# Kernel tuning notes

Measured on AMD Instinct MI355X. Metric: run time of the kernel, lower is better.

The kernel has to match this reference:

```python
import jax, jax.numpy as jnp
import numpy as np

B, S, D, H = 2, 2048, 1024, 16
HD = D // H  # head_dim = 64
LN_EPS = 1e-5


def setup_inputs() -> dict:
    key = jax.random.key(0)
    ks = jax.random.split(key, 14)
    w = 0.02  # weight init scale
    return {
        "q": jax.random.normal(ks[0], (B, S, D), jnp.float32),
        "k": jax.random.normal(ks[1], (B, S, D), jnp.float32),
        "v": jax.random.normal(ks[2], (B, S, D), jnp.float32),
        "mask": jnp.zeros((B, 1, S, S), dtype=bool),
        "training": 0,
        "wq_w": jax.random.normal(ks[3], (D, D), jnp.float32) * w,
        "wq_b": jnp.zeros((D,), jnp.float32),
        "wk_w": jax.random.normal(ks[4], (D, D), jnp.float32) * w,
        "wk_b": jnp.zeros((D,), jnp.float32),
        "wv_w": jax.random.normal(ks[5], (D, D), jnp.float32) * w,
        "wv_b": jnp.zeros((D,), jnp.float32),
        "wo_w": jax.random.normal(ks[6], (D, D), jnp.float32) * w,
        "wo_b": jnp.zeros((D,), jnp.float32),
        "ln_g": jnp.ones((D,), jnp.float32),
        "ln_b": jnp.zeros((D,), jnp.float32),
    }


def _linear(x, w, b):
    # torch nn.Linear: x @ W.T + b, W is [out, in]
    return jnp.einsum('bsd,od->bso', x, w) + b


def _split_heads(x):
    b, s, _ = x.shape
    return x.reshape(b, s, H, HD).transpose(0, 2, 1, 3)  # [B,H,S,HD]


def reference(q, k, v, mask, training, wq_w, wq_b, wk_w, wk_b, wv_w, wv_b,
              wo_w, wo_b, ln_g, ln_b):
    residual = q
    Q = _split_heads(_linear(q, wq_w, wq_b))
    K = _split_heads(_linear(k, wk_w, wk_b))
    V = _split_heads(_linear(v, wv_w, wv_b))
    # source computes sqrt(dk) in float16, then adds 1e-8
    dk = jnp.sqrt(jnp.asarray(HD, jnp.float16)).astype(jnp.float32) + 1e-8
    score = jnp.einsum('bhqd,bhkd->bhqk', Q, K) / dk  # [B,H,S,S]
    # NOTE: source applies NO softmax; masked score is used directly.
    attn = jnp.where(mask, -jnp.inf, score)
    ctx = jnp.einsum('bhqk,bhkd->bhqd', attn, V)  # [B,H,S,HD]
    b, _, s, _ = ctx.shape
    ctx = ctx.transpose(0, 2, 1, 3).reshape(b, s, D)  # [B,S,D]
    o = _linear(ctx, wo_w, wo_b)
    # dropout is identity in eval mode
    x = residual + o
    mu = jnp.mean(x, axis=-1, keepdims=True)
    var = jnp.mean(jnp.square(x - mu), axis=-1, keepdims=True)
    return ln_g * (x - mu) * jax.lax.rsqrt(var + LN_EPS) + ln_b
```

## Files before the change

### kernel.cpp

```cpp
#include <hip/hip_runtime.h>


typedef __bf16 bf16;
typedef __bf16 bf16x8 __attribute__((ext_vector_type(8)));
typedef float f32x4 __attribute__((ext_vector_type(4)));

#define MFMA16(a, b, c) __builtin_amdgcn_mfma_f32_16x16x32_bf16(a, b, c, 0, 0, 0)
#define BARRIER() asm volatile("s_barrier" ::: "memory")
#define VMCNT6() asm volatile("s_waitcnt vmcnt(6)" ::: "memory")
#define VMCNT4() asm volatile("s_waitcnt vmcnt(4)" ::: "memory")
#define VMCNT0() asm volatile("s_waitcnt vmcnt(0)" ::: "memory")
#define LGKM0()                                        \
  do {                                                 \
    asm volatile("s_waitcnt lgkmcnt(0)" ::: "memory"); \
    __builtin_amdgcn_sched_barrier(0);                 \
  } while (0)

__device__ __forceinline__ bf16x8 ld8(const bf16* p) { return *(const bf16x8*)p; }

__device__ __forceinline__ void gload16(const void* g, void* l) {
  __builtin_amdgcn_global_load_lds((__attribute__((address_space(1))) void*)(g),
                                   (__attribute__((address_space(3))) void*)(l), 16, 0, 0);
}

__device__ __forceinline__ int swz4(int row) { return (row ^ (row >> 2)) & 3; }

__global__ __launch_bounds__(256) void wcvt_kernel(
    const float* __restrict__ wq, const float* __restrict__ wk, const float* __restrict__ wv,
    bf16* __restrict__ dst, float* __restrict__ Mz) {
  const int bid = blockIdx.x;
  if (bid >= 1536) {
    float* p = Mz + (size_t)(bid - 1536) * 2048 + threadIdx.x * 8;
    *(f32x4*)p = f32x4{0.f, 0.f, 0.f, 0.f};
    *(f32x4*)(p + 4) = f32x4{0.f, 0.f, 0.f, 0.f};
    return;
  }
  const int y = bid >> 9, x = bid & 511;
  const float* s = (y == 0) ? wq : (y == 1 ? wk : wv);
  const size_t i = ((size_t)x * 256 + threadIdx.x) * 8;
  f32x4 a = *(const f32x4*)(s + i);
  f32x4 b = *(const f32x4*)(s + i + 4);
  bf16x8 o;
  o[0] = (bf16)a[0]; o[1] = (bf16)a[1]; o[2] = (bf16)a[2]; o[3] = (bf16)a[3];
  o[4] = (bf16)b[0]; o[5] = (bf16)b[1]; o[6] = (bf16)b[2]; o[7] = (bf16)b[3];
  *(bf16x8*)(dst + (size_t)y * 1048576u + i) = o;
}

__global__ __launch_bounds__(256, 3) void gemm_proj_a(
    const float* __restrict__ q, const float* __restrict__ k, const float* __restrict__ v,
    const bf16* __restrict__ Wall,
    const float* __restrict__ bq, const float* __restrict__ bk, const float* __restrict__ bv,
    bf16* __restrict__ Call) {
  __shared__ __align__(1024) char lds[49152];
  const int wg = blockIdx.x;
  const int swz = (wg & 7) * 96 + (wg >> 3);
  const int mt = swz >> 3, nt = swz & 7;
  const int z = mt >> 5;
  const int mloc = (mt & 31) * 128;
  const int n0 = nt * 128;
  const float* As = (z == 0) ? q : (z == 1 ? k : v);
  const bf16* W = Wall + (size_t)z * 1048576u + (size_t)n0 * 1024;

  const int t = threadIdx.x;
  const int lane = t & 63, wid = t >> 6;
  const int wr = wid >> 1, wc = wid & 1;
  const int r16 = lane & 15, kg = lane >> 4;

  int aoff[4], boff[4];
#pragma unroll
  for (int i = 0; i < 4; i++) {
    const int arow = wr * 64 + i * 16 + r16;
    aoff[i] = arow * 64 + ((kg ^ swz4(arow)) << 4);
    const int brow = wc * 64 + i * 16 + r16;
    boff[i] = brow * 64 + ((kg ^ swz4(brow)) << 4);
  }

  const int ar = t >> 1;
  const float* Arow = As + (size_t)(mloc + ar) * 1024 + (t & 1) * 16;
  const int ws0 = ar * 64 + (((((t & 1) << 1) | 0) ^ swz4(ar)) << 4);
  const int ws1 = ar * 64 + (((((t & 1) << 1) | 1) ^ swz4(ar)) << 4);

  const int c1 = t, c2 = t + 256;
  const bf16* pb1 = W + (size_t)(c1 >> 2) * 1024 + ((c1 & 3) ^ swz4(c1 >> 2)) * 8;
  const bf16* pb2 = W + (size_t)(c2 >> 2) * 1024 + ((c2 & 3) ^ swz4(c2 >> 2)) * 8;
  const int bd1 = wid << 10, bd2 = 4096 + (wid << 10);

  f32x4 rg0, rg1, rg2, rg3;
  f32x4 acc[4][4] = {};

  {
    const float* p = Arow;
    rg0 = *(const f32x4*)p; rg1 = *(const f32x4*)(p + 4);
    rg2 = *(const f32x4*)(p + 8); rg3 = *(const f32x4*)(p + 12);
  }
  __builtin_amdgcn_sched_barrier(0);
  gload16(pb1, lds + 24576 + bd1);
  gload16(pb2, lds + 24576 + bd2);
  gload16(pb1 + 32, lds + 24576 + 8192 + bd1);
  gload16(pb2 + 32, lds + 24576 + 8192 + bd2);
  {
    bf16x8 p0, p1;
    p0[0] = (bf16)rg0[0]; p0[1] = (bf16)rg0[1]; p0[2] = (bf16)rg0[2]; p0[3] = (bf16)rg0[3];
    p0[4] = (bf16)rg1[0]; p0[5] = (bf16)rg1[1]; p0[6] = (bf16)rg1[2]; p0[7] = (bf16)rg1[3];
    p1[0] = (bf16)rg2[0]; p1[1] = (bf16)rg2[1]; p1[2] = (bf16)rg2[2]; p1[3] = (bf16)rg2[3];
    p1[4] = (bf16)rg3[0]; p1[5] = (bf16)rg3[1]; p1[6] = (bf16)rg3[2]; p1[7] = (bf16)rg3[3];
    *(bf16x8*)(lds + ws0) = p0;
    *(bf16x8*)(lds + ws1) = p1;
  }
  {
    const float* p = Arow + 32;
    rg0 = *(const f32x4*)p; rg1 = *(const f32x4*)(p + 4);
    rg2 = *(const f32x4*)(p + 8); rg3 = *(const f32x4*)(p + 12);
  }
  LGKM0();
  VMCNT6();
  BARRIER();

  int cb = 0;
  for (int kt = 0; kt < 32; ++kt) {
    const char* la = lds + cb * 8192;
    const char* lb = lds + 24576 + cb * 8192;
    bf16x8 av[4], bw[4];
#pragma unroll
    for (int i = 0; i < 4; i++) av[i] = *(const bf16x8*)(la + aoff[i]);
#pragma unroll
    for (int j = 0; j < 4; j++) bw[j] = *(const bf16x8*)(lb + boff[j]);

    const int nb = (cb == 2) ? 0 : cb + 1;
    const int pbuf = (nb == 2) ? 0 : nb + 1;
    if (kt < 31) {
      bf16x8 p0, p1;
      p0[0] = (bf16)rg0[0]; p0[1] = (bf16)rg0[1]; p0[2] = (bf16)rg0[2]; p0[3] = (bf16)rg0[3];
      p0[4] = (bf16)rg1[0]; p0[5] = (bf16)rg1[1]; p0[6] = (bf16)rg1[2]; p0[7] = (bf16)rg1[3];
      p1[0] = (bf16)rg2[0]; p1[1] = (bf16)rg2[1]; p1[2] = (bf16)rg2[2]; p1[3] = (bf16)rg2[3];
      p1[4] = (bf16)rg3[0]; p1[5] = (bf16)rg3[1]; p1[6] = (bf16)rg3[2]; p1[7] = (bf16)rg3[3];
      *(bf16x8*)(lds + nb * 8192 + ws0) = p0;
      *(bf16x8*)(lds + nb * 8192 + ws1) = p1;
    }
    if (kt < 30) {
      const float* p = Arow + (kt + 2) * 32;
      rg0 = *(const f32x4*)p; rg1 = *(const f32x4*)(p + 4);
      rg2 = *(const f32x4*)(p + 8); rg3 = *(const f32x4*)(p + 12);
      __builtin_amdgcn_sched_barrier(0);
      gload16(pb1 + (kt + 2) * 32, lds + 24576 + pbuf * 8192 + bd1);
      gload16(pb2 + (kt + 2) * 32, lds + 24576 + pbuf * 8192 + bd2);
    }
    __builtin_amdgcn_s_setprio(1);
#pragma unroll
    for (int i = 0; i < 4; i++)
#pragma unroll
      for (int j = 0; j < 4; j++) acc[i][j] = MFMA16(av[i], bw[j], acc[i][j]);
    __builtin_amdgcn_s_setprio(0);
    LGKM0();
    if (kt < 30) { VMCNT6(); BARRIER(); }
    else if (kt == 30) { VMCNT0(); BARRIER(); }
    cb = nb;
  }

  const float* bias = (z == 0) ? bq : (z == 1 ? bk : bv);
  bf16* C = Call + (size_t)z * 4194304u;
#pragma unroll
  for (int j = 0; j < 4; j++) {
    const int col = n0 + wc * 64 + j * 16 + r16;
    const float bj = bias[col];
#pragma unroll
    for (int i = 0; i < 4; i++) {
      const int row = mloc + wr * 64 + i * 16 + kg * 4;
#pragma unroll
      for (int r = 0; r < 4; r++)
        C[(size_t)(row + r) * 1024 + col] = (bf16)(acc[i][j][r] + bj);
    }
  }
}

__device__ __forceinline__ void compute16(const char* la, const char* lb,
                                          const int aoff[4], const int boff[4],
                                          f32x4 (&acc)[4][4]) {
  bf16x8 av[4], bv[4];
#pragma unroll
  for (int i = 0; i < 4; i++) av[i] = *(const bf16x8*)(la + aoff[i]);
#pragma unroll
  for (int j = 0; j < 4; j++) bv[j] = *(const bf16x8*)(lb + boff[j]);
  __builtin_amdgcn_s_setprio(1);
#pragma unroll
  for (int i = 0; i < 4; i++)
#pragma unroll
    for (int j = 0; j < 4; j++) acc[i][j] = MFMA16(av[i], bv[j], acc[i][j]);
  __builtin_amdgcn_s_setprio(0);
}

__device__ __forceinline__ void ring128(const bf16* __restrict__ A, const bf16* __restrict__ B,
                                        char* lds, f32x4 (&acc)[4][4]) {
  const int t = threadIdx.x;
  const int lane = t & 63, wid = t >> 6;
  const int wr = wid >> 1, wc = wid & 1;
  const int r16 = lane & 15, kg = lane >> 4;

  int aoff[4], boff[4];
#pragma unroll
  for (int i = 0; i < 4; i++) {
    int row = wr * 64 + i * 16 + r16;
    aoff[i] = row * 64 + ((kg ^ swz4(row)) << 4);
    row = wc * 64 + i * 16 + r16;
    boff[i] = 8192 + row * 64 + ((kg ^ swz4(row)) << 4);
  }

  const int r1 = t >> 2, c = t & 3, r2 = r1 + 64;
  const bf16* pa1 = A + (size_t)r1 * 1024 + (c ^ swz4(r1)) * 8;
  const bf16* pa2 = A + (size_t)r2 * 1024 + (c ^ swz4(r2)) * 8;
  const bf16* pb1 = B + (size_t)r1 * 1024 + (c ^ swz4(r1)) * 8;
  const bf16* pb2 = B + (size_t)r2 * 1024 + (c ^ swz4(r2)) * 8;
  const int d1 = wid << 10, d2 = 4096 + (wid << 10);

#pragma unroll
  for (int p = 0; p < 2; p++) {
    char* d = lds + p * 16384;
    gload16(pa1 + p * 32, d + d1);
    gload16(pa2 + p * 32, d + d2);
    gload16(pb1 + p * 32, d + 8192 + d1);
    gload16(pb2 + p * 32, d + 8192 + d2);
  }
  pa1 += 64; pa2 += 64; pb1 += 64; pb2 += 64;

  int cb = 0, rb = 2;
  for (int kt = 0; kt < 30; kt++) {
    VMCNT4();
    BARRIER();
    {
      char* d = lds + rb * 16384;
      gload16(pa1, d + d1);
      gload16(pa2, d + d2);
      gload16(pb1, d + 8192 + d1);
      gload16(pb2, d + 8192 + d2);
      pa1 += 32; pa2 += 32; pb1 += 32; pb2 += 32;
    }
    compute16(lds + cb * 16384, lds + cb * 16384, aoff, boff, acc);
    LGKM0();
    cb = (cb == 2) ? 0 : cb + 1;
    rb = (rb == 2) ? 0 : rb + 1;
  }
  VMCNT4();
  BARRIER();
  compute16(lds + cb * 16384, lds + cb * 16384, aoff, boff, acc);
  LGKM0();
  cb = (cb == 2) ? 0 : cb + 1;
  VMCNT0(); BARRIER();
  compute16(lds + cb * 16384, lds + cb * 16384, aoff, boff, acc);
}

__global__ __launch_bounds__(256) void ktv_kernel(
    const bf16* __restrict__ Kb, const bf16* __restrict__ Vb, float* __restrict__ M) {
  const int bh = blockIdx.x >> 2, sc = blockIdx.x & 3;
  const int b = bh >> 4, h = bh & 15;
  __shared__ bf16 Kl[64][136];
  __shared__ bf16 Vl[64][136];
  const int t = threadIdx.x;
  const int l = t & 63, w = t >> 6;
  const int r16 = l & 15, kg = l >> 4;
  f32x4 acc[4] = {};
  for (int sub = 0; sub < 4; ++sub) {
    const int s0 = sc * 512 + sub * 128;
    const size_t base = ((size_t)b * 2048 + s0) * 1024 + h * 64;
    if (sub) __syncthreads();
#pragma unroll
    for (int p = 0; p < 4; p++) {
      const int chunk = p * 256 + t;
      const int s = chunk >> 3, d0 = (chunk & 7) * 8;
      bf16x8 kv = ld8(Kb + base + (size_t)s * 1024 + d0);
      bf16x8 vv = ld8(Vb + base + (size_t)s * 1024 + d0);
#pragma unroll
      for (int e = 0; e < 8; e++) { Kl[d0 + e][s] = kv[e]; Vl[d0 + e][s] = vv[e]; }
    }
    __syncthreads();
#pragma unroll
    for (int ks = 0; ks < 4; ks++) {
      bf16x8 a = ld8(&Kl[w * 16 + r16][ks * 32 + kg * 8]);
#pragma unroll
      for (int j = 0; j < 4; j++) {
        bf16x8 bvv = ld8(&Vl[j * 16 + r16][ks * 32 + kg * 8]);
        acc[j] = MFMA16(a, bvv, acc[j]);
      }
    }
  }
  float* Mh = M + (size_t)bh * 4096;
#pragma unroll
  for (int j = 0; j < 4; j++)
#pragma unroll
    for (int r = 0; r < 4; r++)
      atomicAdd(&Mh[(w * 16 + kg * 4 + r) * 64 + j * 16 + r16], acc[j][r]);
}

__global__ __launch_bounds__(256) void gt_kernel(
    const float* __restrict__ Wo, const float* __restrict__ M, bf16* __restrict__ Gt) {
  const int bid = blockIdx.x;
  const int b = bid >> 7, h = (bid >> 3) & 15, nt = bid & 7;
  const int n0 = nt * 128;
  const float* Mh = M + (size_t)((b << 4) + h) * 4096;
  const int l = threadIdx.x & 63, w = threadIdx.x >> 6;
  const int r16 = l & 15, kg = l >> 4;
  f32x4 acc[2][4] = {};
#pragma unroll
  for (int kk = 0; kk < 2; kk++) {
    bf16x8 a[2];
#pragma unroll
    for (int i = 0; i < 2; i++) {
      const float* wp = Wo + (size_t)(n0 + w * 32 + i * 16 + r16) * 1024 + h * 64 + kk * 32 + kg * 8;
      f32x4 lo = *(const f32x4*)wp;
      f32x4 hi = *(const f32x4*)(wp + 4);
      a[i][0] = (bf16)lo[0]; a[i][1] = (bf16)lo[1]; a[i][2] = (bf16)lo[2]; a[i][3] = (bf16)lo[3];
      a[i][4] = (bf16)hi[0]; a[i][5] = (bf16)hi[1]; a[i][6] = (bf16)hi[2]; a[i][7] = (bf16)hi[3];
    }
#pragma unroll
    for (int j = 0; j < 4; j++) {
      const float* mp = Mh + (j * 16 + r16) * 64 + kk * 32 + kg * 8;
      f32x4 m0v = *(const f32x4*)mp;
      f32x4 m1v = *(const f32x4*)(mp + 4);
      bf16x8 bv;
      bv[0] = (bf16)(m0v[0] * 0.125f); bv[1] = (bf16)(m0v[1] * 0.125f);
      bv[2] = (bf16)(m0v[2] * 0.125f); bv[3] = (bf16)(m0v[3] * 0.125f);
      bv[4] = (bf16)(m1v[0] * 0.125f); bv[5] = (bf16)(m1v[1] * 0.125f);
      bv[6] = (bf16)(m1v[2] * 0.125f); bv[7] = (bf16)(m1v[3] * 0.125f);
#pragma unroll
      for (int i = 0; i < 2; i++) acc[i][j] = MFMA16(a[i], bv, acc[i][j]);
    }
  }
  bf16* G = Gt + (size_t)b * 1048576u;
#pragma unroll
  for (int i = 0; i < 2; i++)
#pragma unroll
    for (int j = 0; j < 4; j++)
#pragma unroll
      for (int r = 0; r < 4; r++)
        G[(size_t)(n0 + w * 32 + i * 16 + kg * 4 + r) * 1024 + h * 64 + j * 16 + r16] =
            (bf16)acc[i][j][r];
}

__global__ __launch_bounds__(256, 3) void gemm_out_r(
    const bf16* __restrict__ Q, const bf16* __restrict__ Gt,
    const float* __restrict__ bo, const float* __restrict__ resid, bf16* __restrict__ xb) {
  __shared__ __align__(1024) char lds[49152];
  const int wg = blockIdx.x;
  const int swz = (wg & 7) * 32 + (wg >> 3);
  const int mt = swz >> 3, nt = swz & 7;
  const int m0 = mt * 128, n0 = nt * 128;

  f32x4 acc[4][4] = {};
  ring128(Q + (size_t)m0 * 1024, Gt + (size_t)(m0 >> 11) * 1048576u + (size_t)n0 * 1024, lds, acc);

  const int lane = threadIdx.x & 63, wid = threadIdx.x >> 6;
  const int wr = wid >> 1, wc = wid & 1, r16 = lane & 15, kg = lane >> 4;
#pragma unroll
  for (int j = 0; j < 4; j++) {
    const int col = n0 + wc * 64 + j * 16 + r16;
    const float bj = bo[col];
#pragma unroll
    for (int i = 0; i < 4; i++) {
      const int row = m0 + wr * 64 + i * 16 + kg * 4;
#pragma unroll
      for (int r = 0; r < 4; r++) {
        const size_t off = (size_t)(row + r) * 1024 + col;
        xb[off] = (bf16)(acc[i][j][r] + bj + resid[off]);
      }
    }
  }
}

__global__ __launch_bounds__(256) void ln_kernel(
    const bf16* __restrict__ xb, const float* __restrict__ g, const float* __restrict__ bb,
    float* __restrict__ out) {
  const int lane = threadIdx.x & 63, wid = threadIdx.x >> 6;
  const int row = (blockIdx.x << 2) + wid;
  const bf16* xr = xb + (size_t)row * 1024;
  bf16x8 h0 = ld8(xr + lane * 16);
  bf16x8 h1 = ld8(xr + lane * 16 + 8);
  float v[16];
#pragma unroll
  for (int e = 0; e < 8; e++) { v[e] = (float)h0[e]; v[8 + e] = (float)h1[e]; }
  float s = 0.f, s2 = 0.f;
#pragma unroll
  for (int e = 0; e < 16; e++) { s += v[e]; s2 += v[e] * v[e]; }
#pragma unroll
  for (int m = 32; m; m >>= 1) { s += __shfl_xor(s, m); s2 += __shfl_xor(s2, m); }
  const float mu = s * (1.0f / 1024.0f);
  const float rstd = rsqrtf(s2 * (1.0f / 1024.0f) - mu * mu + 1e-5f);
  float* orow = out + (size_t)row * 1024 + lane * 16;
#pragma unroll
  for (int e = 0; e < 4; e++) {
    f32x4 gg = *(const f32x4*)(g + lane * 16 + e * 4);
    f32x4 bv = *(const f32x4*)(bb + lane * 16 + e * 4);
    f32x4 o;
#pragma unroll
    for (int u = 0; u < 4; u++) o[u] = gg[u] * ((v[e * 4 + u] - mu) * rstd) + bv[u];
    *(f32x4*)(orow + e * 4) = o;
  }
}

extern "C" void kernel_launch(void* const* d_in, const int* in_sizes, int n_in,
                              void* d_out, int out_size, void* d_ws, size_t ws_size,
                              hipStream_t stream) {
  (void)in_sizes; (void)n_in; (void)out_size; (void)ws_size;
  const float* q    = (const float*)d_in[0];
  const float* k    = (const float*)d_in[1];
  const float* v    = (const float*)d_in[2];
  const float* wq_w = (const float*)d_in[5];
  const float* wq_b = (const float*)d_in[6];
  const float* wk_w = (const float*)d_in[7];
  const float* wk_b = (const float*)d_in[8];
  const float* wv_w = (const float*)d_in[9];
  const float* wv_b = (const float*)d_in[10];
  const float* wo_w = (const float*)d_in[11];
  const float* wo_b = (const float*)d_in[12];
  const float* ln_g = (const float*)d_in[13];
  const float* ln_b = (const float*)d_in[14];
  float* out = (float*)d_out;

  bf16* wsb    = (bf16*)d_ws;
  bf16* w_bf   = wsb;
  bf16* QKV_bf = wsb + 3145728u;
  float* M     = (float*)(wsb + 15728640u);
  bf16* Gt     = wsb + 15990784u;
  bf16* xb     = wsb + 18087936u;

  wcvt_kernel<<<1600, 256, 0, stream>>>(wq_w, wk_w, wv_w, w_bf, M);
  gemm_proj_a<<<768, 256, 0, stream>>>(q, k, v, w_bf, wq_b, wk_b, wv_b, QKV_bf);
  ktv_kernel<<<128, 256, 0, stream>>>(QKV_bf + 4194304u, QKV_bf + 8388608u, M);
  gt_kernel<<<256, 256, 0, stream>>>(wo_w, M, Gt);
  gemm_out_r<<<256, 256, 0, stream>>>(QKV_bf, Gt, wo_b, q, xb);
  ln_kernel<<<1024, 256, 0, stream>>>(xb, ln_g, ln_b, out);
}
```

Baseline: 93.02 us.

## Stream fp32 activations straight to LDS and convert to bf16 at fragment load

The projection GEMM now copies the fp32 q/k/v tiles into LDS with direct global-to-LDS loads, where before they went through registers and were converted to bf16 before the LDS store. The bf16 conversion now happens when each thread reads its MFMA fragment from LDS. The aim is to take register staging and conversion off the load path so that A and B prefetch use the same asynchronous mechanism in a three-stage pipeline. In exchange the LDS footprint per block grows to 72KB, occupancy drops from 3 to 2 blocks, and each fragment read doubles its LDS traffic. Other edits are small helper refactors.

New measurement: 97.18 us. 4.5% more time.

```diff
diff --git a/kernel.cpp b/kernel.cpp
--- a/kernel.cpp
+++ b/kernel.cpp
@@ -25,6 +25,13 @@
 
 __device__ __forceinline__ int swz4(int row) { return (row ^ (row >> 2)) & 3; }
 
+__device__ __forceinline__ bf16x8 cvt8(f32x4 lo, f32x4 hi) {
+  bf16x8 o;
+  o[0] = (bf16)lo[0]; o[1] = (bf16)lo[1]; o[2] = (bf16)lo[2]; o[3] = (bf16)lo[3];
+  o[4] = (bf16)hi[0]; o[5] = (bf16)hi[1]; o[6] = (bf16)hi[2]; o[7] = (bf16)hi[3];
+  return o;
+}
+
 __global__ __launch_bounds__(256) void wcvt_kernel(
     const float* __restrict__ wq, const float* __restrict__ wk, const float* __restrict__ wv,
     bf16* __restrict__ dst, float* __restrict__ Mz) {
@@ -38,26 +45,20 @@
   const int y = bid >> 9, x = bid & 511;
   const float* s = (y == 0) ? wq : (y == 1 ? wk : wv);
   const size_t i = ((size_t)x * 256 + threadIdx.x) * 8;
-  f32x4 a = *(const f32x4*)(s + i);
-  f32x4 b = *(const f32x4*)(s + i + 4);
-  bf16x8 o;
-  o[0] = (bf16)a[0]; o[1] = (bf16)a[1]; o[2] = (bf16)a[2]; o[3] = (bf16)a[3];
-  o[4] = (bf16)b[0]; o[5] = (bf16)b[1]; o[6] = (bf16)b[2]; o[7] = (bf16)b[3];
-  *(bf16x8*)(dst + (size_t)y * 1048576u + i) = o;
-}
-
-__global__ __launch_bounds__(256, 3) void gemm_proj_a(
+  *(bf16x8*)(dst + (size_t)y * 1048576u + i) =
+      cvt8(*(const f32x4*)(s + i), *(const f32x4*)(s + i + 4));
+}
+
+__global__ __launch_bounds__(256, 2) void gemm_proj_f32a(
     const float* __restrict__ q, const float* __restrict__ k, const float* __restrict__ v,
     const bf16* __restrict__ Wall,
     const float* __restrict__ bq, const float* __restrict__ bk, const float* __restrict__ bv,
     bf16* __restrict__ Call) {
-  __shared__ __align__(1024) char lds[49152];
+  __shared__ __align__(1024) char lds[73728];
   const int wg = blockIdx.x;
   const int swz = (wg & 7) * 96 + (wg >> 3);
   const int mt = swz >> 3, nt = swz & 7;
-  const int z = mt >> 5;
-  const int mloc = (mt & 31) * 128;
-  const int n0 = nt * 128;
+  const int z = mt >> 5, mloc = (mt & 31) * 128, n0 = nt * 128;
   const float* As = (z == 0) ? q : (z == 1 ? k : v);
   const bf16* W = Wall + (size_t)z * 1048576u + (size_t)n0 * 1024;
 
@@ -70,81 +71,54 @@
 #pragma unroll
   for (int i = 0; i < 4; i++) {
     const int arow = wr * 64 + i * 16 + r16;
-    aoff[i] = arow * 64 + ((kg ^ swz4(arow)) << 4);
+    aoff[i] = arow * 128 + ((kg ^ swz4(arow)) << 5);
     const int brow = wc * 64 + i * 16 + r16;
-    boff[i] = brow * 64 + ((kg ^ swz4(brow)) << 4);
-  }
-
-  const int ar = t >> 1;
-  const float* Arow = As + (size_t)(mloc + ar) * 1024 + (t & 1) * 16;
-  const int ws0 = ar * 64 + (((((t & 1) << 1) | 0) ^ swz4(ar)) << 4);
-  const int ws1 = ar * 64 + (((((t & 1) << 1) | 1) ^ swz4(ar)) << 4);
-
-  const int c1 = t, c2 = t + 256;
-  const bf16* pb1 = W + (size_t)(c1 >> 2) * 1024 + ((c1 & 3) ^ swz4(c1 >> 2)) * 8;
-  const bf16* pb2 = W + (size_t)(c2 >> 2) * 1024 + ((c2 & 3) ^ swz4(c2 >> 2)) * 8;
-  const int bd1 = wid << 10, bd2 = 4096 + (wid << 10);
-
-  f32x4 rg0, rg1, rg2, rg3;
+    boff[i] = 16384 + brow * 64 + ((kg ^ swz4(brow)) << 4);
+  }
+
+  const float* pa[4];
+#pragma unroll
+  for (int p = 0; p < 4; p++) {
+    const int s = p * 256 + t;
+    const int row = s >> 3, c32 = (s & 7) >> 1, half = s & 1;
+    pa[p] = As + (size_t)(mloc + row) * 1024 + ((c32 ^ swz4(row)) << 3) + (half << 2);
+  }
+  const bf16* pb1 = W + (size_t)(t >> 2) * 1024 + (((t & 3) ^ swz4(t >> 2)) << 3);
+  const bf16* pb2 = W + (size_t)((t + 256) >> 2) * 1024 + (((t & 3) ^ swz4((t + 256) >> 2)) << 3);
+  const int widb = wid << 10;
+
   f32x4 acc[4][4] = {};
 
-  {
-    const float* p = Arow;
-    rg0 = *(const f32x4*)p; rg1 = *(const f32x4*)(p + 4);
-    rg2 = *(const f32x4*)(p + 8); rg3 = *(const f32x4*)(p + 12);
-  }
-  __builtin_amdgcn_sched_barrier(0);
-  gload16(pb1, lds + 24576 + bd1);
-  gload16(pb2, lds + 24576 + bd2);
-  gload16(pb1 + 32, lds + 24576 + 8192 + bd1);
-  gload16(pb2 + 32, lds + 24576 + 8192 + bd2);
-  {
-    bf16x8 p0, p1;
-    p0[0] = (bf16)rg0[0]; p0[1] = (bf16)rg0[1]; p0[2] = (bf16)rg0[2]; p0[3] = (bf16)rg0[3];
-    p0[4] = (bf16)rg1[0]; p0[5] = (bf16)rg1[1]; p0[6] = (bf16)rg1[2]; p0[7] = (bf16)rg1[3];
-    p1[0] = (bf16)rg2[0]; p1[1] = (bf16)rg2[1]; p1[2] = (bf16)rg2[2]; p1[3] = (bf16)rg2[3];
-    p1[4] = (bf16)rg3[0]; p1[5] = (bf16)rg3[1]; p1[6] = (bf16)rg3[2]; p1[7] = (bf16)rg3[3];
-    *(bf16x8*)(lds + ws0) = p0;
-    *(bf16x8*)(lds + ws1) = p1;
-  }
-  {
-    const float* p = Arow + 32;
-    rg0 = *(const f32x4*)p; rg1 = *(const f32x4*)(p + 4);
-    rg2 = *(const f32x4*)(p + 8); rg3 = *(const f32x4*)(p + 12);
-  }
-  LGKM0();
-  VMCNT6();
-  BARRIER();
+#pragma unroll
+  for (int kt0 = 0; kt0 < 2; kt0++) {
+    char* d = lds + kt0 * 24576;
+#pragma unroll
+    for (int p = 0; p < 4; p++) gload16(pa[p] + kt0 * 32, d + p * 4096 + widb);
+    gload16(pb1 + kt0 * 32, d + 16384 + widb);
+    gload16(pb2 + kt0 * 32, d + 16384 + 4096 + widb);
+  }
 
   int cb = 0;
   for (int kt = 0; kt < 32; ++kt) {
-    const char* la = lds + cb * 8192;
-    const char* lb = lds + 24576 + cb * 8192;
+    if (kt < 30) VMCNT6(); else if (kt == 30) VMCNT6(); else VMCNT0();
+    BARRIER();
+    if (kt < 30) {
+      char* d = lds + ((kt + 2) % 3) * 24576;
+#pragma unroll
+      for (int p = 0; p < 4; p++) gload16(pa[p] + (kt + 2) * 32, d + p * 4096 + widb);
+      gload16(pb1 + (kt + 2) * 32, d + 16384 + widb);
+      gload16(pb2 + (kt + 2) * 32, d + 16384 + 4096 + widb);
+    }
+    const char* buf = lds + cb * 24576;
     bf16x8 av[4], bw[4];
 #pragma unroll
-    for (int i = 0; i < 4; i++) av[i] = *(const bf16x8*)(la + aoff[i]);
-#pragma unroll
-    for (int j = 0; j < 4; j++) bw[j] = *(const bf16x8*)(lb + boff[j]);
-
-    const int nb = (cb == 2) ? 0 : cb + 1;
-    const int pbuf = (nb == 2) ? 0 : nb + 1;
-    if (kt < 31) {
-      bf16x8 p0, p1;
-      p0[0] = (bf16)rg0[0]; p0[1] = (bf16)rg0[1]; p0[2] = (bf16)rg0[2]; p0[3] = (bf16)rg0[3];
-      p0[4] = (bf16)rg1[0]; p0[5] = (bf16)rg1[1]; p0[6] = (bf16)rg1[2]; p0[7] = (bf16)rg1[3];
-      p1[0] = (bf16)rg2[0]; p1[1] = (bf16)rg2[1]; p1[2] = (bf16)rg2[2]; p1[3] = (bf16)rg2[3];
-      p1[4] = (bf16)rg3[0]; p1[5] = (bf16)rg3[1]; p1[6] = (bf16)rg3[2]; p1[7] = (bf16)rg3[3];
-      *(bf16x8*)(lds + nb * 8192 + ws0) = p0;
-      *(bf16x8*)(lds + nb * 8192 + ws1) = p1;
-    }
-    if (kt < 30) {
-      const float* p = Arow + (kt + 2) * 32;
-      rg0 = *(const f32x4*)p; rg1 = *(const f32x4*)(p + 4);
-      rg2 = *(const f32x4*)(p + 8); rg3 = *(const f32x4*)(p + 12);
-      __builtin_amdgcn_sched_barrier(0);
-      gload16(pb1 + (kt + 2) * 32, lds + 24576 + pbuf * 8192 + bd1);
-      gload16(pb2 + (kt + 2) * 32, lds + 24576 + pbuf * 8192 + bd2);
-    }
+    for (int i = 0; i < 4; i++) {
+      f32x4 lo = *(const f32x4*)(buf + aoff[i]);
+      f32x4 hi = *(const f32x4*)(buf + aoff[i] + 16);
+      av[i] = cvt8(lo, hi);
+    }
+#pragma unroll
+    for (int j = 0; j < 4; j++) bw[j] = *(const bf16x8*)(buf + boff[j]);
     __builtin_amdgcn_s_setprio(1);
 #pragma unroll
     for (int i = 0; i < 4; i++)
@@ -152,9 +126,7 @@
       for (int j = 0; j < 4; j++) acc[i][j] = MFMA16(av[i], bw[j], acc[i][j]);
     __builtin_amdgcn_s_setprio(0);
     LGKM0();
-    if (kt < 30) { VMCNT6(); BARRIER(); }
-    else if (kt == 30) { VMCNT0(); BARRIER(); }
-    cb = nb;
+    cb = (cb == 2) ? 0 : cb + 1;
   }
 
   const float* bias = (z == 0) ? bq : (z == 1 ? bk : bv);
@@ -173,14 +145,13 @@
   }
 }
 
-__device__ __forceinline__ void compute16(const char* la, const char* lb,
-                                          const int aoff[4], const int boff[4],
+__device__ __forceinline__ void compute16(const char* buf, const int aoff[4], const int boff[4],
                                           f32x4 (&acc)[4][4]) {
   bf16x8 av[4], bv[4];
 #pragma unroll
-  for (int i = 0; i < 4; i++) av[i] = *(const bf16x8*)(la + aoff[i]);
-#pragma unroll
-  for (int j = 0; j < 4; j++) bv[j] = *(const bf16x8*)(lb + boff[j]);
+  for (int i = 0; i < 4; i++) av[i] = *(const bf16x8*)(buf + aoff[i]);
+#pragma unroll
+  for (int j = 0; j < 4; j++) bv[j] = *(const bf16x8*)(buf + boff[j]);
   __builtin_amdgcn_s_setprio(1);
 #pragma unroll
   for (int i = 0; i < 4; i++)
@@ -234,18 +205,18 @@
       gload16(pb2, d + 8192 + d2);
       pa1 += 32; pa2 += 32; pb1 += 32; pb2 += 32;
     }
-    compute16(lds + cb * 16384, lds + cb * 16384, aoff, boff, acc);
+    compute16(lds + cb * 16384, aoff, boff, acc);
     LGKM0();
     cb = (cb == 2) ? 0 : cb + 1;
     rb = (rb == 2) ? 0 : rb + 1;
   }
   VMCNT4();
   BARRIER();
-  compute16(lds + cb * 16384, lds + cb * 16384, aoff, boff, acc);
+  compute16(lds + cb * 16384, aoff, boff, acc);
   LGKM0();
   cb = (cb == 2) ? 0 : cb + 1;
   VMCNT0(); BARRIER();
-  compute16(lds + cb * 16384, lds + cb * 16384, aoff, boff, acc);
+  compute16(lds + cb * 16384, aoff, boff, acc);
 }
 
 __global__ __launch_bounds__(256) void ktv_kernel(
@@ -305,21 +276,16 @@
 #pragma unroll
     for (int i = 0; i < 2; i++) {
       const float* wp = Wo + (size_t)(n0 + w * 32 + i * 16 + r16) * 1024 + h * 64 + kk * 32 + kg * 8;
-      f32x4 lo = *(const f32x4*)wp;
-      f32x4 hi = *(const f32x4*)(wp + 4);
-      a[i][0] = (bf16)lo[0]; a[i][1] = (bf16)lo[1]; a[i][2] = (bf16)lo[2]; a[i][3] = (bf16)lo[3];
-      a[i][4] = (bf16)hi[0]; a[i][5] = (bf16)hi[1]; a[i][6] = (bf16)hi[2]; a[i][7] = (bf16)hi[3];
+      a[i] = cvt8(*(const f32x4*)wp, *(const f32x4*)(wp + 4));
     }
 #pragma unroll
     for (int j = 0; j < 4; j++) {
       const float* mp = Mh + (j * 16 + r16) * 64 + kk * 32 + kg * 8;
       f32x4 m0v = *(const f32x4*)mp;
       f32x4 m1v = *(const f32x4*)(mp + 4);
-      bf16x8 bv;
-      bv[0] = (bf16)(m0v[0] * 0.125f); bv[1] = (bf16)(m0v[1] * 0.125f);
-      bv[2] = (bf16)(m0v[2] * 0.125f); bv[3] = (bf16)(m0v[3] * 0.125f);
-      bv[4] = (bf16)(m1v[0] * 0.125f); bv[5] = (bf16)(m1v[1] * 0.125f);
-      bv[6] = (bf16)(m1v[2] * 0.125f); bv[7] = (bf16)(m1v[3] * 0.125f);
+      f32x4 sl = {m0v[0] * 0.125f, m0v[1] * 0.125f, m0v[2] * 0.125f, m0v[3] * 0.125f};
+      f32x4 sh = {m1v[0] * 0.125f, m1v[1] * 0.125f, m1v[2] * 0.125f, m1v[3] * 0.125f};
+      bf16x8 bv = cvt8(sl, sh);
 #pragma unroll
       for (int i = 0; i < 2; i++) acc[i][j] = MFMA16(a[i], bv, acc[i][j]);
     }
@@ -422,7 +388,7 @@
   bf16* xb     = wsb + 18087936u;
 
   wcvt_kernel<<<1600, 256, 0, stream>>>(wq_w, wk_w, wv_w, w_bf, M);
-  gemm_proj_a<<<768, 256, 0, stream>>>(q, k, v, w_bf, wq_b, wk_b, wv_b, QKV_bf);
+  gemm_proj_f32a<<<768, 256, 0, stream>>>(q, k, v, w_bf, wq_b, wk_b, wv_b, QKV_bf);
   ktv_kernel<<<128, 256, 0, stream>>>(QKV_bf + 4194304u, QKV_bf + 8388608u, M);
   gt_kernel<<<256, 256, 0, stream>>>(wo_w, M, Gt);
   gemm_out_r<<<256, 256, 0, stream>>>(QKV_bf, Gt, wo_b, q, xb);
```
